# Performance work log

Measured on AMD Instinct MI355X. Metric: run time of the kernel, lower is better.

The kernel has to match this reference:

```python
import jax, jax.numpy as jnp
import numpy as np

N_NODES = 50000
N_EDGES = 800000
D_IN = 128
D_HID = 128
D_OUT = 128


def setup_inputs() -> dict:
    key = jax.random.key(0)
    ks = jax.random.split(key, 10)
    x = jax.random.normal(ks[0], (N_NODES, D_IN), dtype=jnp.float32)
    edge_index = jax.random.randint(ks[1], (2, N_EDGES), 0, N_NODES, dtype=jnp.int64)
    edge_index_inter = jax.random.randint(ks[2], (2, N_EDGES), 0, N_NODES, dtype=jnp.int64)
    # nn.Linear-style params: W [out, in], b [out]
    def linear(k, fan_in, fan_out):
        k1, k2 = jax.random.split(k)
        bound = 1.0 / np.sqrt(fan_in)
        W = jax.random.uniform(k1, (fan_out, fan_in), minval=-bound, maxval=bound, dtype=jnp.float32)
        b = jax.random.uniform(k2, (fan_out,), minval=-bound, maxval=bound, dtype=jnp.float32)
        return W, b
    W1, b1 = linear(ks[3], D_IN, D_HID)
    W2, b2 = linear(ks[4], D_HID, D_HID)
    W3, b3 = linear(ks[5], D_HID, D_OUT)
    return {"x": x, "W1": W1, "b1": b1, "W2": W2, "b2": b2, "W3": W3, "b3": b3,
            "edge_index": edge_index, "edge_index_inter": edge_index_inter}


def _gnn_layer(h, W, b, src, dst, n_nodes):
    # message: lin(x_j - x_i); x_j = source features, x_i = target features (PyG convention)
    msg = (h[src] - h[dst]) @ W.T + b          # [E, out]
    # aggr='add': scatter-add messages into target nodes
    return jax.ops.segment_sum(msg, dst, num_segments=n_nodes)  # [N, out]


def reference(x, W1, b1, W2, b2, W3, b3, edge_index, edge_index_inter):
    src, dst = edge_index[0], edge_index[1]
    n = x.shape[0]
    h = _gnn_layer(x, W1, b1, src, dst, n)
    h = _gnn_layer(h, W2, b2, src, dst, n)
    return _gnn_layer(h, W3, b3, src, dst, n)
```

## Files before the change

kernel.cpp:

```cpp
#include <hip/hip_runtime.h>

#define N_NODES 50000
#define N_EDGES 800000
#define D 128
#define TN 16
#define TSTR 136
#define SCAN_BLOCKS 196

typedef __attribute__((ext_vector_type(8))) short bf16x8;
typedef __attribute__((ext_vector_type(4))) float f32x4;

__device__ __forceinline__ unsigned short f32_to_bf16_rne(float f) {
    unsigned u = __float_as_uint(f);
    u += 0x7fffu + ((u >> 16) & 1u);
    return (unsigned short)(u >> 16);
}

__device__ __forceinline__ float bflo(unsigned u) { return __uint_as_float(u << 16); }
__device__ __forceinline__ float bfhi(unsigned u) { return __uint_as_float(u & 0xffff0000u); }

__device__ __forceinline__ void acc8(uint4 r, float* a) {
    a[0] += bflo(r.x); a[1] += bfhi(r.x);
    a[2] += bflo(r.y); a[3] += bfhi(r.y);
    a[4] += bflo(r.z); a[5] += bfhi(r.z);
    a[6] += bflo(r.w); a[7] += bfhi(r.w);
}

template <int U>
__device__ __forceinline__ void gather16(const unsigned short* __restrict__ hb,
                                         int myidx, int i, int rowid2, int d8,
                                         float* a0, float* a1) {
    int si[U];
    uint4 rr[U];
#pragma unroll
    for (int u = 0; u < U; ++u) si[u] = __shfl(myidx, i + 2 * u + rowid2, 32);
#pragma unroll
    for (int u = 0; u < U; ++u) rr[u] = *(const uint4*)(hb + (size_t)si[u] * D + 8 * d8);
#pragma unroll
    for (int u = 0; u < U; ++u) acc8(rr[u], (u & 1) ? a1 : a0);
}

__device__ __forceinline__ void gather_node(const unsigned short* __restrict__ hb,
                                            const unsigned short* __restrict__ esrc,
                                            int beg, int deg, int idx0,
                                            int l32, int rowid2, int d8,
                                            float* out) {
    float a0[8] = {0.f, 0.f, 0.f, 0.f, 0.f, 0.f, 0.f, 0.f};
    float a1[8] = {0.f, 0.f, 0.f, 0.f, 0.f, 0.f, 0.f, 0.f};
    int myidx = idx0;
    int base = 0;
    while (true) {
        const int cnt = min(deg - base, 32);
        int i = 0;
        for (; i + 16 <= cnt; i += 16) gather16<8>(hb, myidx, i, rowid2, d8, a0, a1);
        if (i + 8 <= cnt) { gather16<4>(hb, myidx, i, rowid2, d8, a0, a1); i += 8; }
        if (i + 4 <= cnt) { gather16<2>(hb, myidx, i, rowid2, d8, a0, a1); i += 4; }
        if (i + 2 <= cnt) { gather16<1>(hb, myidx, i, rowid2, d8, a0, a1); i += 2; }
        if (i < cnt) {
            const int s0 = __shfl(myidx, i, 32);
            if (rowid2 == 0) {
                const uint4 r = *(const uint4*)(hb + (size_t)s0 * D + 8 * d8);
                acc8(r, a0);
            }
        }
        base += 32;
        if (base >= deg) break;
        myidx = 0;
        if (l32 < deg - base) myidx = (int)esrc[beg + base + l32];
    }
#pragma unroll
    for (int k = 0; k < 8; ++k) {
        float s = a0[k] + a1[k];
        s += __shfl_xor(s, 16, 64);
        out[k] = s;
    }
}

__global__ void prep_kernel(const int* __restrict__ dst, int* __restrict__ counts,
                            unsigned short* __restrict__ rank,
                            const float* __restrict__ x, unsigned short* __restrict__ xb) {
    const int t = blockIdx.x * blockDim.x + threadIdx.x;
    if (t < N_EDGES) {
        rank[t] = (unsigned short)atomicAdd(&counts[dst[t]], 1);
    }
    {
        const float4 v0 = *(const float4*)(x + (size_t)t * 8);
        const float4 v1 = *(const float4*)(x + (size_t)t * 8 + 4);
        uint4 p;
        p.x = (unsigned)f32_to_bf16_rne(v0.x) | ((unsigned)f32_to_bf16_rne(v0.y) << 16);
        p.y = (unsigned)f32_to_bf16_rne(v0.z) | ((unsigned)f32_to_bf16_rne(v0.w) << 16);
        p.z = (unsigned)f32_to_bf16_rne(v1.x) | ((unsigned)f32_to_bf16_rne(v1.y) << 16);
        p.w = (unsigned)f32_to_bf16_rne(v1.z) | ((unsigned)f32_to_bf16_rne(v1.w) << 16);
        *(uint4*)(xb + (size_t)t * 8) = p;
    }
}

__global__ void block_sum_kernel(const int* __restrict__ counts, int* __restrict__ bsum) {
    __shared__ int red[256];
    const int tid = threadIdx.x;
    const int i = blockIdx.x * 256 + tid;
    red[tid] = (i < N_NODES) ? counts[i] : 0;
    __syncthreads();
    for (int s = 128; s > 0; s >>= 1) {
        if (tid < s) red[tid] += red[tid + s];
        __syncthreads();
    }
    if (tid == 0) bsum[blockIdx.x] = red[0];
}

__global__ void bsum_scan_kernel(const int* __restrict__ bsum,
                                 int* __restrict__ bpre,
                                 int* __restrict__ offsets) {
    __shared__ int s[256];
    const int tid = threadIdx.x;
    const int v = (tid < SCAN_BLOCKS) ? bsum[tid] : 0;
    s[tid] = v;
    __syncthreads();
    for (int off = 1; off < 256; off <<= 1) {
        int a = (tid >= off) ? s[tid - off] : 0;
        __syncthreads();
        s[tid] += a;
        __syncthreads();
    }
    bpre[tid] = s[tid] - v;
    if (tid == 255) offsets[N_NODES] = s[255];
}

__global__ void offsets_wfrag_kernel(const int* __restrict__ counts,
                                     const int* __restrict__ bpre,
                                     int* __restrict__ offsets,
                                     const float* __restrict__ W1,
                                     const float* __restrict__ W2,
                                     const float* __restrict__ W3,
                                     unsigned short* __restrict__ Wb) {
    if (blockIdx.x < SCAN_BLOCKS) {
        __shared__ int s[256];
        const int tid = threadIdx.x;
        const int i = blockIdx.x * 256 + tid;
        const int v = (i < N_NODES) ? counts[i] : 0;
        s[tid] = v;
        __syncthreads();
        for (int off = 1; off < 256; off <<= 1) {
            int a = (tid >= off) ? s[tid - off] : 0;
            __syncthreads();
            s[tid] += a;
            __syncthreads();
        }
        const int excl = s[tid] - v + bpre[blockIdx.x];
        if (i < N_NODES) offsets[i] = excl;
    } else {
        const int unit = (blockIdx.x - SCAN_BLOCKS) * 2 + (threadIdx.x >> 7);
        const int w = unit >> 7;
        const int o = unit & 127;
        const int k = threadIdx.x & 127;
        const float* W = (w == 0) ? W1 : (w == 1) ? W2 : W3;
        const unsigned short v = f32_to_bf16_rne(W[o * D + k]);
        const int nt = o >> 4, n = o & 15;
        const int kc = k >> 5, kr = k & 31, quad = kr >> 3, j = kr & 7;
        const int lane = quad * 16 + n;
        Wb[(((size_t)w * 8 + nt) * 4 + kc) * 512 + lane * 8 + j] = v;
    }
}

__global__ void fill_kernel(const int* __restrict__ src, const int* __restrict__ dst,
                            const unsigned short* __restrict__ rank,
                            const int* __restrict__ offsets,
                            unsigned short* __restrict__ esrc) {
    int e = blockIdx.x * blockDim.x + threadIdx.x;
    if (e < N_EDGES) {
        esrc[offsets[dst[e]] + (int)rank[e]] = (unsigned short)src[e];
    }
}

template <bool OUT_BF16>
__global__ __launch_bounds__(256) void gnn_layer_kernel(
    const unsigned short* __restrict__ hb,
    const int* __restrict__ offsets,
    const unsigned short* __restrict__ esrc,
    const unsigned short* __restrict__ Wb,
    const float* __restrict__ bias,
    float* __restrict__ outf,
    unsigned short* __restrict__ outb) {

    __shared__ __align__(16) unsigned short tb[TN][TSTR];
    __shared__ float degf[TN];

    const int tid = threadIdx.x;
    const int wave = tid >> 6;
    const int lane = tid & 63;
    const int half = lane >> 5;
    const int l32 = lane & 31;
    const int rowid2 = (lane >> 4) & 1;
    const int d8 = lane & 15;
    const int vbase = blockIdx.x * TN;

    const int j0 = wave * 4 + half * 2;
    const int v0 = vbase + j0;

    const int begA = offsets[v0];
    const int begB = offsets[v0 + 1];
    const int degA = begB - begA;
    const int degB = offsets[v0 + 2] - begB;

    int idxA = 0, idxB = 0;
    if (l32 < min(degA, 32)) idxA = (int)esrc[begA + l32];
    if (l32 < min(degB, 32)) idxB = (int)esrc[begB + l32];

    float sA[8], sB[8];
    gather_node(hb, esrc, begA, degA, idxA, l32, rowid2, d8, sA);
    gather_node(hb, esrc, begB, degB, idxB, l32, rowid2, d8, sB);

    {
        const int vv = v0 + rowid2;
        const float dv = (float)(rowid2 ? degB : degA);
        const uint4 r = *(const uint4*)(hb + (size_t)vv * D + 8 * d8);
        float t[8];
#pragma unroll
        for (int k = 0; k < 8; ++k) t[k] = rowid2 ? sB[k] : sA[k];
        t[0] -= dv * bflo(r.x); t[1] -= dv * bfhi(r.x);
        t[2] -= dv * bflo(r.y); t[3] -= dv * bfhi(r.y);
        t[4] -= dv * bflo(r.z); t[5] -= dv * bfhi(r.z);
        t[6] -= dv * bflo(r.w); t[7] -= dv * bfhi(r.w);
        uint4 p;
        p.x = (unsigned)f32_to_bf16_rne(t[0]) | ((unsigned)f32_to_bf16_rne(t[1]) << 16);
        p.y = (unsigned)f32_to_bf16_rne(t[2]) | ((unsigned)f32_to_bf16_rne(t[3]) << 16);
        p.z = (unsigned)f32_to_bf16_rne(t[4]) | ((unsigned)f32_to_bf16_rne(t[5]) << 16);
        p.w = (unsigned)f32_to_bf16_rne(t[6]) | ((unsigned)f32_to_bf16_rne(t[7]) << 16);
        *(uint4*)&tb[j0 + rowid2][8 * d8] = p;
        if (d8 == 0) degf[j0 + rowid2] = dv;
    }
    __syncthreads();

    const int n16 = lane & 15;
    const int quad = lane >> 4;

    bf16x8 afrag[4];
#pragma unroll
    for (int kc = 0; kc < 4; ++kc)
        afrag[kc] = *(const bf16x8*)&tb[n16][kc * 32 + quad * 8];

#pragma unroll
    for (int i = 0; i < 2; ++i) {
        const int nt = wave * 2 + i;
        f32x4 acc = {0.f, 0.f, 0.f, 0.f};
#pragma unroll
        for (int kc = 0; kc < 4; ++kc) {
            const bf16x8 bfrag = *(const bf16x8*)&Wb[((nt * 4 + kc) * 64 + lane) * 8];
            acc = __builtin_amdgcn_mfma_f32_16x16x32_bf16(afrag[kc], bfrag, acc, 0, 0, 0);
        }
        const int o = nt * 16 + n16;
        const float bo = bias[o];
#pragma unroll
        for (int r = 0; r < 4; ++r) {
            const int m = quad * 4 + r;
            const float val = acc[r] + degf[m] * bo;
            if (OUT_BF16)
                outb[(size_t)(vbase + m) * D + o] = f32_to_bf16_rne(val);
            else
                outf[(size_t)(vbase + m) * D + o] = val;
        }
    }
}

extern "C" void kernel_launch(void* const* d_in, const int* in_sizes, int n_in,
                              void* d_out, int out_size, void* d_ws, size_t ws_size,
                              hipStream_t stream) {
    const float* x  = (const float*)d_in[0];
    const float* W1 = (const float*)d_in[1];
    const float* b1 = (const float*)d_in[2];
    const float* W2 = (const float*)d_in[3];
    const float* b2 = (const float*)d_in[4];
    const float* W3 = (const float*)d_in[5];
    const float* b3 = (const float*)d_in[6];
    const int*   ei = (const int*)d_in[7];

    const int* src = ei;
    const int* dst = ei + N_EDGES;
    float* out = (float*)d_out;

    char* ws = (char*)d_ws;
    int* counts  = (int*)ws;                          ws += 204800;
    int* offsets = (int*)ws;                          ws += 204800;
    int* bsum    = (int*)ws;                          ws += 1024;
    int* bpre    = (int*)ws;                          ws += 1024;
    unsigned short* rank = (unsigned short*)ws;       ws += (size_t)N_EDGES * 2;
    unsigned short* esrc = (unsigned short*)ws;       ws += (size_t)N_EDGES * 2;
    unsigned short* Wb = (unsigned short*)ws;         ws += 3 * 16384 * 2;
    unsigned short* xb = (unsigned short*)ws;         ws += (size_t)N_NODES * D * 2;
    unsigned short* h1 = (unsigned short*)ws;         ws += (size_t)N_NODES * D * 2;
    unsigned short* h2 = (unsigned short*)ws;

    hipMemsetAsync(counts, 0, N_NODES * sizeof(int), stream);
    prep_kernel<<<(N_EDGES + 255) / 256, 256, 0, stream>>>(dst, counts, rank, x, xb);
    block_sum_kernel<<<SCAN_BLOCKS, 256, 0, stream>>>(counts, bsum);
    bsum_scan_kernel<<<1, 256, 0, stream>>>(bsum, bpre, offsets);
    offsets_wfrag_kernel<<<SCAN_BLOCKS + 192, 256, 0, stream>>>(counts, bpre, offsets,
                                                                W1, W2, W3, Wb);
    fill_kernel<<<(N_EDGES + 255) / 256, 256, 0, stream>>>(src, dst, rank, offsets, esrc);

    const int blocks = N_NODES / TN;

    gnn_layer_kernel<true ><<<blocks, 256, 0, stream>>>(xb, offsets, esrc, Wb,          b1, nullptr, h1);
    gnn_layer_kernel<true ><<<blocks, 256, 0, stream>>>(h1, offsets, esrc, Wb + 16384,  b2, nullptr, h2);
    gnn_layer_kernel<false><<<blocks, 256, 0, stream>>>(h2, offsets, esrc, Wb + 32768,  b3, out, nullptr);
}
```

Baseline: 252.7 us.

## Pad gathers with a zero row and halve the nodes per block

Each layout slab gets an extra all-zero feature row, written once in the prep kernel. Neighbour lists can then be padded to a multiple of 16 indices with that row, which removes the branchy tail handling (8/4/2/1 cases) in the gather loop. The layer kernel also moves to 8 nodes per 128-thread block, which doubles the block count for more parallelism. In exchange, the MFMA still runs on a 16-row tile with half its rows unused, and low-degree nodes issue extra loads of the zero row.

```diff
diff --git a/kernel.cpp b/kernel.cpp
--- a/kernel.cpp
+++ b/kernel.cpp
@@ -3,9 +3,10 @@
 #define N_NODES 50000
 #define N_EDGES 800000
 #define D 128
-#define TN 16
+#define TN 8
 #define TSTR 136
 #define SCAN_BLOCKS 196
+#define ZROW N_NODES
 
 typedef __attribute__((ext_vector_type(8))) short bf16x8;
 typedef __attribute__((ext_vector_type(4))) float f32x4;
@@ -26,18 +27,17 @@
     a[6] += bflo(r.w); a[7] += bfhi(r.w);
 }
 
-template <int U>
-__device__ __forceinline__ void gather16(const unsigned short* __restrict__ hb,
-                                         int myidx, int i, int rowid2, int d8,
-                                         float* a0, float* a1) {
-    int si[U];
-    uint4 rr[U];
-#pragma unroll
-    for (int u = 0; u < U; ++u) si[u] = __shfl(myidx, i + 2 * u + rowid2, 32);
-#pragma unroll
-    for (int u = 0; u < U; ++u) rr[u] = *(const uint4*)(hb + (size_t)si[u] * D + 8 * d8);
-#pragma unroll
-    for (int u = 0; u < U; ++u) acc8(rr[u], (u & 1) ? a1 : a0);
+__device__ __forceinline__ void gather16x8(const unsigned short* __restrict__ hb,
+                                           int myidx, int i, int rowid2, int d8,
+                                           float* a0, float* a1) {
+    int si[8];
+    uint4 rr[8];
+#pragma unroll
+    for (int u = 0; u < 8; ++u) si[u] = __shfl(myidx, i + 2 * u + rowid2, 32);
+#pragma unroll
+    for (int u = 0; u < 8; ++u) rr[u] = *(const uint4*)(hb + (size_t)si[u] * D + 8 * d8);
+#pragma unroll
+    for (int u = 0; u < 8; ++u) acc8(rr[u], (u & 1) ? a1 : a0);
 }
 
 __device__ __forceinline__ void gather_node(const unsigned short* __restrict__ hb,
@@ -51,21 +51,11 @@
     int base = 0;
     while (true) {
         const int cnt = min(deg - base, 32);
-        int i = 0;
-        for (; i + 16 <= cnt; i += 16) gather16<8>(hb, myidx, i, rowid2, d8, a0, a1);
-        if (i + 8 <= cnt) { gather16<4>(hb, myidx, i, rowid2, d8, a0, a1); i += 8; }
-        if (i + 4 <= cnt) { gather16<2>(hb, myidx, i, rowid2, d8, a0, a1); i += 4; }
-        if (i + 2 <= cnt) { gather16<1>(hb, myidx, i, rowid2, d8, a0, a1); i += 2; }
-        if (i < cnt) {
-            const int s0 = __shfl(myidx, i, 32);
-            if (rowid2 == 0) {
-                const uint4 r = *(const uint4*)(hb + (size_t)s0 * D + 8 * d8);
-                acc8(r, a0);
-            }
-        }
+        for (int i = 0; i < cnt; i += 16)
+            gather16x8(hb, myidx, i, rowid2, d8, a0, a1);
         base += 32;
         if (base >= deg) break;
-        myidx = 0;
+        myidx = ZROW;
         if (l32 < deg - base) myidx = (int)esrc[beg + base + l32];
     }
 #pragma unroll
@@ -78,7 +68,8 @@
 
 __global__ void prep_kernel(const int* __restrict__ dst, int* __restrict__ counts,
                             unsigned short* __restrict__ rank,
-                            const float* __restrict__ x, unsigned short* __restrict__ xb) {
+                            const float* __restrict__ x, unsigned short* __restrict__ xb,
+                            unsigned short* __restrict__ h1, unsigned short* __restrict__ h2) {
     const int t = blockIdx.x * blockDim.x + threadIdx.x;
     if (t < N_EDGES) {
         rank[t] = (unsigned short)atomicAdd(&counts[dst[t]], 1);
@@ -92,6 +83,12 @@
         p.z = (unsigned)f32_to_bf16_rne(v1.x) | ((unsigned)f32_to_bf16_rne(v1.y) << 16);
         p.w = (unsigned)f32_to_bf16_rne(v1.z) | ((unsigned)f32_to_bf16_rne(v1.w) << 16);
         *(uint4*)(xb + (size_t)t * 8) = p;
+    }
+    if (blockIdx.x == 0 && threadIdx.x < 48) {
+        const int rowsel = threadIdx.x >> 4;
+        const int off = threadIdx.x & 15;
+        unsigned short* zp = (rowsel == 0) ? xb : (rowsel == 1) ? h1 : h2;
+        *(uint4*)(zp + (size_t)ZROW * D + off * 8) = make_uint4(0u, 0u, 0u, 0u);
     }
 }
 
@@ -173,7 +170,7 @@
 }
 
 template <bool OUT_BF16>
-__global__ __launch_bounds__(256) void gnn_layer_kernel(
+__global__ __launch_bounds__(128) void gnn_layer_kernel(
     const unsigned short* __restrict__ hb,
     const int* __restrict__ offsets,
     const unsigned short* __restrict__ esrc,
@@ -182,7 +179,7 @@
     float* __restrict__ outf,
     unsigned short* __restrict__ outb) {
 
-    __shared__ __align__(16) unsigned short tb[TN][TSTR];
+    __shared__ __align__(16) unsigned short tb[16][TSTR];
     __shared__ float degf[TN];
 
     const int tid = threadIdx.x;
@@ -202,7 +199,7 @@
     const int degA = begB - begA;
     const int degB = offsets[v0 + 2] - begB;
 
-    int idxA = 0, idxB = 0;
+    int idxA = ZROW, idxB = ZROW;
     if (l32 < min(degA, 32)) idxA = (int)esrc[begA + l32];
     if (l32 < min(degB, 32)) idxB = (int)esrc[begB + l32];
 
@@ -240,24 +237,26 @@
         afrag[kc] = *(const bf16x8*)&tb[n16][kc * 32 + quad * 8];
 
 #pragma unroll
-    for (int i = 0; i < 2; ++i) {
-        const int nt = wave * 2 + i;
+    for (int i = 0; i < 4; ++i) {
+        const int nt = wave * 4 + i;
         f32x4 acc = {0.f, 0.f, 0.f, 0.f};
 #pragma unroll
         for (int kc = 0; kc < 4; ++kc) {
             const bf16x8 bfrag = *(const bf16x8*)&Wb[((nt * 4 + kc) * 64 + lane) * 8];
             acc = __builtin_amdgcn_mfma_f32_16x16x32_bf16(afrag[kc], bfrag, acc, 0, 0, 0);
         }
-        const int o = nt * 16 + n16;
-        const float bo = bias[o];
-#pragma unroll
-        for (int r = 0; r < 4; ++r) {
-            const int m = quad * 4 + r;
-            const float val = acc[r] + degf[m] * bo;
-            if (OUT_BF16)
-                outb[(size_t)(vbase + m) * D + o] = f32_to_bf16_rne(val);
-            else
-                outf[(size_t)(vbase + m) * D + o] = val;
+        if (quad < 2) {
+            const int o = nt * 16 + n16;
+            const float bo = bias[o];
+#pragma unroll
+            for (int r = 0; r < 4; ++r) {
+                const int m = quad * 4 + r;
+                const float val = acc[r] + degf[m] * bo;
+                if (OUT_BF16)
+                    outb[(size_t)(vbase + m) * D + o] = f32_to_bf16_rne(val);
+                else
+                    outf[(size_t)(vbase + m) * D + o] = val;
+            }
         }
     }
 }
@@ -278,6 +277,7 @@
     const int* dst = ei + N_EDGES;
     float* out = (float*)d_out;
 
+    const size_t HSLAB = (size_t)(N_NODES + 2) * D * 2;
     char* ws = (char*)d_ws;
     int* counts  = (int*)ws;                          ws += 204800;
     int* offsets = (int*)ws;                          ws += 204800;
@@ -286,12 +286,12 @@
     unsigned short* rank = (unsigned short*)ws;       ws += (size_t)N_EDGES * 2;
     unsigned short* esrc = (unsigned short*)ws;       ws += (size_t)N_EDGES * 2;
     unsigned short* Wb = (unsigned short*)ws;         ws += 3 * 16384 * 2;
-    unsigned short* xb = (unsigned short*)ws;         ws += (size_t)N_NODES * D * 2;
-    unsigned short* h1 = (unsigned short*)ws;         ws += (size_t)N_NODES * D * 2;
+    unsigned short* xb = (unsigned short*)ws;         ws += HSLAB;
+    unsigned short* h1 = (unsigned short*)ws;         ws += HSLAB;
     unsigned short* h2 = (unsigned short*)ws;
 
     hipMemsetAsync(counts, 0, N_NODES * sizeof(int), stream);
-    prep_kernel<<<(N_EDGES + 255) / 256, 256, 0, stream>>>(dst, counts, rank, x, xb);
+    prep_kernel<<<(N_EDGES + 255) / 256, 256, 0, stream>>>(dst, counts, rank, x, xb, h1, h2);
     block_sum_kernel<<<SCAN_BLOCKS, 256, 0, stream>>>(counts, bsum);
     bsum_scan_kernel<<<1, 256, 0, stream>>>(bsum, bpre, offsets);
     offsets_wfrag_kernel<<<SCAN_BLOCKS + 192, 256, 0, stream>>>(counts, bpre, offsets,
@@ -300,7 +300,7 @@
 
     const int blocks = N_NODES / TN;
 
-    gnn_layer_kernel<true ><<<blocks, 256, 0, stream>>>(xb, offsets, esrc, Wb,          b1, nullptr, h1);
-    gnn_layer_kernel<true ><<<blocks, 256, 0, stream>>>(h1, offsets, esrc, Wb + 16384,  b2, nullptr, h2);
-    gnn_layer_kernel<false><<<blocks, 256, 0, stream>>>(h2, offsets, esrc, Wb + 32768,  b3, out, nullptr);
-}
+    gnn_layer_kernel<true ><<<blocks, 128, 0, stream>>>(xb, offsets, esrc, Wb,          b1, nullptr, h1);
+    gnn_layer_kernel<true ><<<blocks, 128, 0, stream>>>(h1, offsets, esrc, Wb + 16384,  b2, nullptr, h2);
+    gnn_layer_kernel<false><<<blocks, 128, 0, stream>>>(h2, offsets, esrc, Wb + 32768,  b3, out, nullptr);
+}
```

New measurement: 254.6 us. Within noise of the previous version (+0.8%).
